# Kernel optimization log

Measured on AMD Instinct MI355X. Metric: run time of the kernel, lower is better.

The kernel has to match this reference:

```python
import jax, jax.numpy as jnp
import numpy as np
import math

B, S = 1, 2048
HID = 4096
NH = 32            # total query heads
NKV = 8            # total kv heads
D = HID // NH      # 128 head_dim
WIN = 1024         # sliding window (layer_idx=1 is odd and < num_layers//2)
LAYER = 1
THETA = 10000.0
LAMBDA_INIT = 0.8 - 0.6 * math.exp(-0.3 * LAYER)
SCALE = D ** -0.5
EPS = 1e-5
OP = NH * D + 2 * NKV * D  # Wqkv output size


def setup_inputs() -> dict:
    key = jax.random.key(0)
    ks = jax.random.split(key, 9)
    std = 0.02
    return {
        "hidden_states": jax.random.normal(ks[0], (B * S, HID), jnp.float32),
        "positions": jnp.tile(jnp.arange(S, dtype=jnp.int32), B),
        "Wqkv_w": jax.random.normal(ks[1], (OP, HID), jnp.float32) * std,
        "Wqkv_b": jnp.zeros((OP,), jnp.float32),
        "out_w": jax.random.normal(ks[2], (HID, NH * D), jnp.float32) * std,
        "out_b": jnp.zeros((HID,), jnp.float32),
        "lambda_q1": jax.random.normal(ks[3], (D,), jnp.float32) * 0.1,
        "lambda_k1": jax.random.normal(ks[4], (D,), jnp.float32) * 0.1,
        "lambda_q2": jax.random.normal(ks[5], (D,), jnp.float32) * 0.1,
        "lambda_k2": jax.random.normal(ks[6], (D,), jnp.float32) * 0.1,
        "subln_w": jnp.ones((2 * D,), jnp.float32),
    }


def _rope(x, pos):
    # neox-style rotary; x: [N, H, D], pos: [N]
    half = D // 2
    inv_freq = 1.0 / (THETA ** (jnp.arange(half, dtype=jnp.float32) / half))
    ang = pos.astype(jnp.float32)[:, None] * inv_freq[None, :]      # [N, half]
    cos = jnp.cos(ang)[:, None, :]
    sin = jnp.sin(ang)[:, None, :]
    x1, x2 = x[..., :half], x[..., half:]
    return jnp.concatenate([x1 * cos - x2 * sin, x2 * cos + x1 * sin], axis=-1)


def _probs(q, k, mask):
    # q: [B,S,Hq,D], k: [B,S,Hkv,D] -> softmax probs [B,Hq,S,S] with GQA repeat
    g = q.shape[2] // k.shape[2]
    k = jnp.repeat(k, g, axis=2)
    scores = jnp.einsum('bqhd,bkhd->bhqk', q, k) * SCALE
    scores = jnp.where(mask, scores, -1e30)
    return jax.nn.softmax(scores, axis=-1)


def _pv(p, v, g):
    # p: [B,Hq,S,S], v: [B,S,Hkv,D]
    v = jnp.repeat(v, g, axis=2)
    return jnp.einsum('bhqk,bkhd->bqhd', p, v)


def reference(hidden_states, positions, Wqkv_w, Wqkv_b, out_w, out_b,
              lambda_q1, lambda_k1, lambda_q2, lambda_k2, subln_w):
    qkv = hidden_states @ Wqkv_w.T + Wqkv_b                 # [N, OP]
    q, k, v = jnp.split(qkv, [NH * D, NH * D + NKV * D], axis=-1)
    q = q.reshape(-1, NH, D)
    k = k.reshape(-1, NKV, D)
    v = v.reshape(-1, NKV, D)
    q = _rope(q, positions)
    k = _rope(k, positions)

    q = q.reshape(B, S, NH, D)
    k = k.reshape(B, S, NKV, D)
    v = v.reshape(B, S, NKV, D)
    # split_heads: '(H two) D' -> even heads = group1, odd heads = group2
    q1, q2 = q[:, :, 0::2], q[:, :, 1::2]
    k1, k2 = k[:, :, 0::2], k[:, :, 1::2]
    v1, v2 = v[:, :, 0::2], v[:, :, 1::2]

    i = jnp.arange(S)[:, None]
    j = jnp.arange(S)[None, :]
    mask = (j <= i) & ((i - j) < WIN)                        # causal + sliding window

    g = (NH // 2) // (NKV // 2)
    p1 = _probs(q1, k1, mask)
    p2 = _probs(q2, k2, mask)
    a11 = _pv(p1, v1, g)
    a12 = _pv(p1, v2, g)
    a21 = _pv(p2, v1, g)
    a22 = _pv(p2, v2, g)

    attn1 = jnp.concatenate([a11, a12], axis=-1)             # [B,S,NH/2,2D]
    attn2 = jnp.concatenate([a21, a22], axis=-1)

    lam = (jnp.exp(jnp.sum(lambda_q1 * lambda_k1))
           - jnp.exp(jnp.sum(lambda_q2 * lambda_k2)) + LAMBDA_INIT)
    attn = attn1 - lam * attn2

    # subln: RMSNorm over last dim (2*head_dim)
    var = jnp.mean(attn * attn, axis=-1, keepdims=True)
    attn = attn * jax.lax.rsqrt(var + EPS) * subln_w
    attn = attn * (1.0 - LAMBDA_INIT)

    attn = attn.reshape(B * S, NH * D)
    return attn @ out_w.T + out_b
```

## Files before the change

### kernel.cpp

```cpp
#include <hip/hip_runtime.h>

typedef unsigned short u16;
typedef __attribute__((ext_vector_type(8))) short bf16x8;
typedef __attribute__((ext_vector_type(4))) float f32x4;
typedef __attribute__((ext_vector_type(4))) unsigned short us4;
typedef __attribute__((ext_vector_type(8))) unsigned short us8;

#define S_LEN 2048
#define QKV_P 6144
#define WIN_SZ 1024
#define SCALE_F 0.08838834764831845f
#define LAMBDA_INIT_F 0.35550906759096925f
#define ONE_MINUS_LI_F 0.6444909324090308f

__device__ __forceinline__ u16 f2bf(float f) {
    union { float f; unsigned int u; } v; v.f = f;
    unsigned int u = v.u;
    return (u16)((u + 0x7fffu + ((u >> 16) & 1u)) >> 16);
}
__device__ __forceinline__ float bf2f(u16 u) {
    union { unsigned int u; float f; } v; v.u = ((unsigned int)u) << 16; return v.f;
}
__device__ __forceinline__ void gload16(const void* g, void* l) {
    __builtin_amdgcn_global_load_lds(
        (const __attribute__((address_space(1))) unsigned int*)g,
        (__attribute__((address_space(3))) unsigned int*)l, 16, 0, 0);
}

__global__ __launch_bounds__(256)
void conv_f32_bf16(const float* __restrict__ src, u16* __restrict__ dst, int n4) {
    for (int i = blockIdx.x * 256 + threadIdx.x; i < n4; i += gridDim.x * 256) {
        float4 v = ((const float4*)src)[i];
        us4 h;
        h.x = f2bf(v.x); h.y = f2bf(v.y); h.z = f2bf(v.z); h.w = f2bf(v.w);
        ((us4*)dst)[i] = h;
    }
}

template<int NR>
__device__ __forceinline__ void stage_half(const u16* __restrict__ src, int K,
                                           int gRowBase, int kcol0,
                                           u16* slot, int tid, int wid) {
#pragma unroll
    for (int g = 0; g < 2; ++g) {
        if (g * 128 + wid * 16 < NR) {
            int row = g * 128 + (tid >> 2);
            int cc = (tid & 3) ^ ((row >> 1) & 3);
            gload16(src + (size_t)(gRowBase + row) * K + kcol0 + cc * 8,
                    slot + g * 4096 + wid * 512);
        }
    }
}

__device__ __forceinline__ bf16x8 ldfrag(const u16* slot, int row, int l4) {
    int pc = l4 ^ ((row >> 1) & 3);
    return *(const bf16x8*)(slot + row * 32 + pc * 8);
}

template<int NF>
__device__ __forceinline__ void gemm_wait(int wid) {
    if constexpr (NF == 3) {
        if (wid < 4) asm volatile("s_waitcnt vmcnt(4)" ::: "memory");
        else         asm volatile("s_waitcnt vmcnt(3)" ::: "memory");
    } else if constexpr (NF == 2) {
        asm volatile("s_waitcnt vmcnt(3)" ::: "memory");
    } else {
        asm volatile("s_waitcnt vmcnt(4)" ::: "memory");
    }
}

template<int NF, int OUT_BF16>
__global__ __launch_bounds__(512)
__attribute__((amdgpu_waves_per_eu(2, 2)))
void gemm8p(const u16* __restrict__ A, const u16* __restrict__ W,
            const float* __restrict__ bias, void* __restrict__ Cv,
            int M, int N, int K, int nbx) {
    constexpr int BN = NF * 64;
    constexpr int BSLOT = NF * 2048;
    __shared__ u16 lds[32768 + 4 * BSLOT];

    const int tid = threadIdx.x;
    const int wid = tid >> 6, lane = tid & 63;
    const int wr = wid >> 2, wc = wid & 3;
    const int l15 = lane & 15, l4 = lane >> 4;

    const int nwg = gridDim.x;
    const int q8 = nwg >> 3;
    const int swz = (blockIdx.x & 7) * q8 + (blockIdx.x >> 3);
    const int bx = swz % nbx, by = swz / nbx;
    const int rowBase = by * 256;
    const int colBase = bx * BN;

    const int NT = K >> 6;

    u16* const baseA = lds;
    u16* const baseB = lds + 32768;

    f32x4 acc[8][NF] = {};

    stage_half<256>(A, K, rowBase, 0,  baseA + 0 * 8192, tid, wid);
    stage_half<BN> (W, K, colBase, 0,  baseB + 0 * BSLOT, tid, wid);
    stage_half<256>(A, K, rowBase, 32, baseA + 1 * 8192, tid, wid);
    stage_half<BN> (W, K, colBase, 32, baseB + 1 * BSLOT, tid, wid);
    stage_half<256>(A, K, rowBase, 64, baseA + 2 * 8192, tid, wid);
    stage_half<BN> (W, K, colBase, 64, baseB + 2 * BSLOT, tid, wid);
    gemm_wait<NF>(wid);
    __builtin_amdgcn_s_barrier();

    for (int t = 0; t < NT; ++t) {
        const int b = t & 1;
        const int bn = b ^ 1;
        u16* const A0 = baseA + (b * 2 + 0) * 8192;
        u16* const A1 = baseA + (b * 2 + 1) * 8192;
        u16* const B0 = baseB + (b * 2 + 0) * BSLOT;
        u16* const B1 = baseB + (b * 2 + 1) * BSLOT;

        bf16x8 af[4], bfv[NF];

#pragma unroll
        for (int m = 0; m < 4; ++m) af[m] = ldfrag(A0, wr * 128 + m * 16 + l15, l4);
#pragma unroll
        for (int n = 0; n < NF; ++n) bfv[n] = ldfrag(B0, wc * (NF * 16) + n * 16 + l15, l4);
        if (t + 1 < NT)
            stage_half<256>(A, K, rowBase, (t + 1) * 64 + 32, baseA + (bn * 2 + 1) * 8192, tid, wid);
        __builtin_amdgcn_s_barrier();
        __builtin_amdgcn_s_setprio(1);
#pragma unroll
        for (int m = 0; m < 4; ++m)
#pragma unroll
            for (int n = 0; n < NF; ++n)
                acc[m][n] = __builtin_amdgcn_mfma_f32_16x16x32_bf16(af[m], bfv[n], acc[m][n], 0, 0, 0);
        __builtin_amdgcn_s_setprio(0);
        __builtin_amdgcn_s_barrier();

#pragma unroll
        for (int m = 0; m < 4; ++m) af[m] = ldfrag(A0, wr * 128 + (m + 4) * 16 + l15, l4);
        if (t + 1 < NT)
            stage_half<BN>(W, K, colBase, (t + 1) * 64 + 32, baseB + (bn * 2 + 1) * BSLOT, tid, wid);
        __builtin_amdgcn_s_barrier();
        __builtin_amdgcn_s_setprio(1);
#pragma unroll
        for (int m = 0; m < 4; ++m)
#pragma unroll
            for (int n = 0; n < NF; ++n)
                acc[m + 4][n] = __builtin_amdgcn_mfma_f32_16x16x32_bf16(af[m], bfv[n], acc[m + 4][n], 0, 0, 0);
        __builtin_amdgcn_s_setprio(0);
        __builtin_amdgcn_s_barrier();

#pragma unroll
        for (int m = 0; m < 4; ++m) af[m] = ldfrag(A1, wr * 128 + m * 16 + l15, l4);
#pragma unroll
        for (int n = 0; n < NF; ++n) bfv[n] = ldfrag(B1, wc * (NF * 16) + n * 16 + l15, l4);
        if (t + 2 < NT)
            stage_half<256>(A, K, rowBase, (t + 2) * 64, baseA + (b * 2 + 0) * 8192, tid, wid);
        __builtin_amdgcn_s_barrier();
        __builtin_amdgcn_s_setprio(1);
#pragma unroll
        for (int m = 0; m < 4; ++m)
#pragma unroll
            for (int n = 0; n < NF; ++n)
                acc[m][n] = __builtin_amdgcn_mfma_f32_16x16x32_bf16(af[m], bfv[n], acc[m][n], 0, 0, 0);
        __builtin_amdgcn_s_setprio(0);
        __builtin_amdgcn_s_barrier();

#pragma unroll
        for (int m = 0; m < 4; ++m) af[m] = ldfrag(A1, wr * 128 + (m + 4) * 16 + l15, l4);
        if (t + 2 < NT)
            stage_half<BN>(W, K, colBase, (t + 2) * 64, baseB + (b * 2 + 0) * BSLOT, tid, wid);
        __builtin_amdgcn_s_barrier();
        __builtin_amdgcn_s_setprio(1);
#pragma unroll
        for (int m = 0; m < 4; ++m)
#pragma unroll
            for (int n = 0; n < NF; ++n)
                acc[m + 4][n] = __builtin_amdgcn_mfma_f32_16x16x32_bf16(af[m], bfv[n], acc[m + 4][n], 0, 0, 0);
        __builtin_amdgcn_s_setprio(0);
        if (t + 2 < NT) gemm_wait<NF>(wid);
        else            asm volatile("s_waitcnt vmcnt(0)" ::: "memory");
        __builtin_amdgcn_s_barrier();
    }

#pragma unroll
    for (int n = 0; n < NF; ++n) {
        int col = colBase + wc * (NF * 16) + n * 16 + l15;
        float bs = bias[col];
#pragma unroll
        for (int m = 0; m < 8; ++m)
#pragma unroll
            for (int rr = 0; rr < 4; ++rr) {
                int rowi = rowBase + wr * 128 + m * 16 + l4 * 4 + rr;
                float v = acc[m][n][rr] + bs;
                if (OUT_BF16) ((u16*)Cv)[(size_t)rowi * N + col] = f2bf(v);
                else          ((float*)Cv)[(size_t)rowi * N + col] = v;
            }
    }
}

__global__ __launch_bounds__(256)
void rope_bf16(u16* __restrict__ qkv, const int* __restrict__ positions) {
    const int row = blockIdx.x;
    const float pos = (float)positions[row];
    for (int idx = threadIdx.x; idx < 640; idx += 256) {
        int head = idx >> 4;
        int g = idx & 15;
        int base = (head < 32) ? head * 128 : 4096 + (head - 32) * 128;
        u16* p = qkv + (size_t)row * QKV_P + base + g * 4;
        us4 x1 = *(us4*)p;
        us4 x2 = *(us4*)(p + 64);
#pragma unroll
        for (int j = 0; j < 4; ++j) {
            float inv_freq = __expf(-(float)(g * 4 + j) * (9.210340371976184f / 64.0f));
            float ang = pos * inv_freq;
            float s, c;
            sincosf(ang, &s, &c);
            float a = bf2f(x1[j]), b = bf2f(x2[j]);
            x1[j] = f2bf(a * c - b * s);
            x2[j] = f2bf(b * c + a * s);
        }
        *(us4*)p = x1;
        *(us4*)(p + 64) = x2;
    }
}

__global__ __launch_bounds__(256)
void vtrans(const u16* __restrict__ qkv, u16* __restrict__ vt) {
    __shared__ u16 T[128 * 72];
    const int s0 = blockIdx.x * 64;
    const int a = blockIdx.y;
    const u16* src = qkv + 5120 + a * 128;
#pragma unroll
    for (int it = 0; it < 4; ++it) {
        int idx = it * 256 + threadIdx.x;
        int s = idx >> 4;
        int c8 = idx & 15;
        us8 v = *(const us8*)(src + (size_t)(s0 + s) * QKV_P + c8 * 8);
        int sc = s >> 3, su = s & 7;
#pragma unroll
        for (int j = 0; j < 8; ++j) {
            int d = c8 * 8 + j;
            T[d * 72 + ((sc ^ ((d >> 3) & 7)) * 8 + su)] = v[j];
        }
    }
    __syncthreads();
#pragma unroll
    for (int it = 0; it < 4; ++it) {
        int idx = it * 256 + threadIdx.x;
        int d = idx >> 3, sc = idx & 7;
        us8 v = *(const us8*)&T[d * 72 + ((sc ^ ((d >> 3) & 7)) * 8)];
        *(us8*)(vt + (size_t)a * 262144 + (size_t)d * 2048 + s0 + sc * 8) = v;
    }
}

__global__ __launch_bounds__(512)
__attribute__((amdgpu_waves_per_eu(2, 2)))
void attn_bf16(const u16* __restrict__ qkv, const u16* __restrict__ vtg,
               u16* __restrict__ attnb,
               const float* __restrict__ lq1, const float* __restrict__ lk1,
               const float* __restrict__ lq2, const float* __restrict__ lk2,
               const float* __restrict__ subln) {
    __shared__ u16 smem[73728];
#define KBUF(b, st) (smem + ((b) * 2 + (st)) * 8192)
#define VBUF(b, st) (smem + 32768 + ((b) * 2 + (st)) * 8192)

    const int tid = threadIdx.x;
    const int w = tid >> 6, lane = tid & 63;
    const int g = w & 3, sid = w >> 2;
    const int l15 = lane & 15, l4 = lane >> 4;
    u16* const Pw = smem + 65536 + w * 1024;

    int qb, h;
    {
        int i = blockIdx.x;
        if (i < 256) { qb = 16 + (i & 15); h = i >> 4; }
        else         { int j = i - 256; qb = j & 15; h = j >> 4; }
    }
    const int q0 = qb * 64;
    const int a1 = 2 * (h >> 2), a2 = a1 + 1;

    bf16x8 qf[4];
    {
        int qrow = q0 + g * 16 + l15;
        const u16* qp = qkv + (size_t)qrow * QKV_P + (2 * h + sid) * 128;
#pragma unroll
        for (int kk = 0; kk < 4; ++kk)
            qf[kk] = *(const bf16x8*)(qp + kk * 32 + l4 * 8);
    }

    f32x4 aV1[8] = {}, aV2[8] = {};
    float m[4], l[4];
#pragma unroll
    for (int r = 0; r < 4; ++r) { m[r] = -1e30f; l[r] = 0.f; }

    const int kr4 = lane >> 4, kc = lane & 15;
    const int vd8 = lane >> 3, vc = lane & 7;

    const int tbeg = (qb >= 16) ? (qb - 16) : 0;
    const int tend = qb;

#define STAGE_TILE(T, NB)                                                      \
    {                                                                          \
        const int kv0s = (T) * 64;                                             \
        _Pragma("unroll")                                                      \
        for (int s2 = 0; s2 < 2; ++s2) {                                       \
            int ch = w * 2 + s2;                                               \
            int krow = ch * 4 + kr4;                                           \
            int kcs = (kc ^ (krow & 7)) * 8;                                   \
            const u16* kbase = qkv + (size_t)(kv0s + krow) * QKV_P + 4096;     \
            gload16(kbase + a1 * 128 + kcs, KBUF(NB, 0) + ch * 512);           \
            gload16(kbase + a2 * 128 + kcs, KBUF(NB, 1) + ch * 512);           \
            int vdrow = ch * 8 + vd8;                                          \
            int vcs = (vc ^ (vdrow & 7)) * 8;                                  \
            const u16* vbase = vtg + (size_t)vdrow * 2048 + kv0s + vcs;        \
            gload16(vbase + (size_t)a1 * 262144, VBUF(NB, 0) + ch * 512);      \
            gload16(vbase + (size_t)a2 * 262144, VBUF(NB, 1) + ch * 512);      \
        }                                                                      \
    }

    STAGE_TILE(tbeg, 0);
    asm volatile("s_waitcnt vmcnt(0)" ::: "memory");
    __builtin_amdgcn_s_barrier();
    asm volatile("" ::: "memory");

    int cb = 0;
    for (int t = tbeg; t <= tend; ++t) {
        const int kv0 = t * 64;

        if (t < tend) STAGE_TILE(t + 1, cb ^ 1);

        f32x4 sc[4];
        const u16* Kc = KBUF(cb, sid);
        __builtin_amdgcn_s_setprio(1);
#pragma unroll
        for (int c = 0; c < 4; ++c) {
            f32x4 s1 = {0.f, 0.f, 0.f, 0.f};
#pragma unroll
            for (int kk = 0; kk < 4; ++kk) {
                int off = (c * 16 + l15) * 128 + (((kk * 4 + l4) ^ (l15 & 7)) * 8);
                s1 = __builtin_amdgcn_mfma_f32_16x16x32_bf16(qf[kk], *(const bf16x8*)&Kc[off], s1, 0, 0, 0);
            }
            sc[c] = s1;
        }
        __builtin_amdgcn_s_setprio(0);

        const bool dz = (t == tend);
        const bool wz = (qb >= 16) && (t <= tbeg + 1);
        if (dz) {
#pragma unroll
            for (int c = 0; c < 4; ++c) {
                int j = kv0 + c * 16 + l15;
#pragma unroll
                for (int r = 0; r < 4; ++r) {
                    int i = q0 + g * 16 + l4 * 4 + r;
                    if (j > i) sc[c][r] = -1e30f;
                }
            }
        } else if (wz) {
#pragma unroll
            for (int c = 0; c < 4; ++c) {
                int j = kv0 + c * 16 + l15;
#pragma unroll
                for (int r = 0; r < 4; ++r) {
                    int i = q0 + g * 16 + l4 * 4 + r;
                    if (i - j >= WIN_SZ) sc[c][r] = -1e30f;
                }
            }
        }

        float rmax[4];
#pragma unroll
        for (int r = 0; r < 4; ++r)
            rmax[r] = fmaxf(fmaxf(sc[0][r], sc[1][r]), fmaxf(sc[2][r], sc[3][r]));
#pragma unroll
        for (int msk = 1; msk < 16; msk <<= 1)
#pragma unroll
            for (int r = 0; r < 4; ++r)
                rmax[r] = fmaxf(rmax[r], __shfl_xor(rmax[r], msk));
        bool need = false;
#pragma unroll
        for (int r = 0; r < 4; ++r)
            need = need || (rmax[r] > m[r] + 32.0f);
        if (__any(need)) {
            float fr[4];
#pragma unroll
            for (int r = 0; r < 4; ++r) {
                float nm = fmaxf(m[r], rmax[r]);
                fr[r] = __expf((m[r] - nm) * SCALE_F);
                m[r] = nm;
                l[r] *= fr[r];
            }
#pragma unroll
            for (int f = 0; f < 8; ++f)
#pragma unroll
                for (int r = 0; r < 4; ++r) {
                    aV1[f][r] *= fr[r];
                    aV2[f][r] *= fr[r];
                }
        }

        float rs[4] = {0.f, 0.f, 0.f, 0.f};
#pragma unroll
        for (int c = 0; c < 4; ++c) {
            int col = c * 16 + l15;
#pragma unroll
            for (int r = 0; r < 4; ++r) {
                int prow = l4 * 4 + r;
                float p = __expf((sc[c][r] - m[r]) * SCALE_F);
                if (wz && (m[r] < -1e29f)) p = 0.f;
                rs[r] += p;
                int pco = ((col >> 3) ^ (prow & 7)) * 8 + (col & 7);
                Pw[prow * 64 + pco] = f2bf(p);
            }
        }
#pragma unroll
        for (int msk = 1; msk < 16; msk <<= 1)
#pragma unroll
            for (int r = 0; r < 4; ++r)
                rs[r] += __shfl_xor(rs[r], msk);
#pragma unroll
        for (int r = 0; r < 4; ++r) l[r] += rs[r];

        const u16* V0 = VBUF(cb, 0);
        const u16* V1 = VBUF(cb, 1);
        __builtin_amdgcn_s_setprio(1);
#pragma unroll
        for (int kk = 0; kk < 2; ++kk) {
            int pch = ((kk * 4 + l4) ^ (l15 & 7)) * 8;
            bf16x8 pa = *(const bf16x8*)&Pw[l15 * 64 + pch];
#pragma unroll
            for (int f = 0; f < 8; ++f) {
                int off = (f * 16 + l15) * 64 + (((kk * 4 + l4) ^ (l15 & 7)) * 8);
                aV1[f] = __builtin_amdgcn_mfma_f32_16x16x32_bf16(pa, *(const bf16x8*)&V0[off], aV1[f], 0, 0, 0);
                aV2[f] = __builtin_amdgcn_mfma_f32_16x16x32_bf16(pa, *(const bf16x8*)&V1[off], aV2[f], 0, 0, 0);
            }
        }
        __builtin_amdgcn_s_setprio(0);

        asm volatile("s_waitcnt vmcnt(0)" ::: "memory");
        __builtin_amdgcn_s_barrier();
        asm volatile("" ::: "memory");
        cb ^= 1;
    }

    float s1v = lq1[lane] * lk1[lane] + lq1[lane + 64] * lk1[lane + 64];
    float s2v = lq2[lane] * lk2[lane] + lq2[lane + 64] * lk2[lane + 64];
#pragma unroll
    for (int msk = 1; msk < 64; msk <<= 1) {
        s1v += __shfl_xor(s1v, msk);
        s2v += __shfl_xor(s2v, msk);
    }
    const float lam = __expf(s1v) - __expf(s2v) + LAMBDA_INIT_F;

    float* const Cmb = (float*)smem;
    if (sid == 1) {
#pragma unroll
        for (int r = 0; r < 4; ++r) {
            float inv2 = lam / l[r];
            int row = g * 16 + l4 * 4 + r;
#pragma unroll
            for (int f = 0; f < 8; ++f) {
                Cmb[row * 264 + f * 16 + l15]       = aV1[f][r] * inv2;
                Cmb[row * 264 + 128 + f * 16 + l15] = aV2[f][r] * inv2;
            }
        }
    }
    __syncthreads();
    if (sid == 0) {
        float sw0[8], sw1[8];
#pragma unroll
        for (int f = 0; f < 8; ++f) {
            sw0[f] = subln[f * 16 + l15];
            sw1[f] = subln[128 + f * 16 + l15];
        }
#pragma unroll
        for (int r = 0; r < 4; ++r) {
            float inv1 = 1.0f / l[r];
            int row = g * 16 + l4 * 4 + r;
            float o0[8], o1[8];
            float ssq = 0.f;
#pragma unroll
            for (int f = 0; f < 8; ++f) {
                o0[f] = aV1[f][r] * inv1 - Cmb[row * 264 + f * 16 + l15];
                o1[f] = aV2[f][r] * inv1 - Cmb[row * 264 + 128 + f * 16 + l15];
                ssq += o0[f] * o0[f] + o1[f] * o1[f];
            }
#pragma unroll
            for (int msk = 1; msk < 16; msk <<= 1) ssq += __shfl_xor(ssq, msk);
            float scale = rsqrtf(ssq * (1.0f / 256.0f) + 1e-5f) * ONE_MINUS_LI_F;
            u16* op = attnb + (size_t)(q0 + row) * 4096 + h * 256;
#pragma unroll
            for (int f = 0; f < 8; ++f) {
                op[f * 16 + l15]       = f2bf(o0[f] * scale * sw0[f]);
                op[128 + f * 16 + l15] = f2bf(o1[f] * scale * sw1[f]);
            }
        }
    }
#undef STAGE_TILE
#undef KBUF
#undef VBUF
}

extern "C" void kernel_launch(void* const* d_in, const int* in_sizes, int n_in,
                              void* d_out, int out_size, void* d_ws, size_t ws_size,
                              hipStream_t stream) {
    const float* hidden    = (const float*)d_in[0];
    const int*   positions = (const int*)d_in[1];
    const float* Wqkv_w    = (const float*)d_in[2];
    const float* Wqkv_b    = (const float*)d_in[3];
    const float* out_w     = (const float*)d_in[4];
    const float* out_b     = (const float*)d_in[5];
    const float* lq1       = (const float*)d_in[6];
    const float* lk1       = (const float*)d_in[7];
    const float* lq2       = (const float*)d_in[8];
    const float* lk2       = (const float*)d_in[9];
    const float* subln     = (const float*)d_in[10];
    float* out = (float*)d_out;

    u16* ws0   = (u16*)d_ws;
    u16* hb    = ws0;
    u16* wqb   = ws0 + 8388608;
    u16* qkvb  = ws0 + 33554432;
    u16* attnb = ws0;
    u16* owb   = ws0 + 8388608;
    u16* vt    = ws0 + 25165824;

    conv_f32_bf16<<<2048, 256, 0, stream>>>(hidden, hb, 2048 * 4096 / 4);
    conv_f32_bf16<<<2048, 256, 0, stream>>>(Wqkv_w, wqb, 6144 * 4096 / 4);

    gemm8p<3, 1><<<256, 512, 0, stream>>>(hb, wqb, Wqkv_b, qkvb, 2048, 6144, 4096, 32);

    rope_bf16<<<S_LEN, 256, 0, stream>>>(qkvb, positions);
    vtrans<<<dim3(32, 8), 256, 0, stream>>>(qkvb, vt);

    conv_f32_bf16<<<2048, 256, 0, stream>>>(out_w, owb, 4096 * 4096 / 4);

    attn_bf16<<<512, 512, 0, stream>>>(qkvb, vt, attnb, lq1, lk1, lq2, lk2, subln);

    gemm8p<2, 0><<<256, 512, 0, stream>>>(attnb, owb, out_b, out, 2048, 4096, 4096, 32);
}
```

Baseline: 362.9 us.

## Halve attention KV tile to 32 rows to cut LDS and raise occupancy

Shrinks the KV tile processed per iteration from 64 to 32 keys. This halves the shared-memory footprint (K/V double buffers and P scratch) and drops the fixed two-waves-per-EU attribute, so more workgroups can be resident per CU. The LDS swizzle patterns, staging addresses, mask boundaries and PV loop are reworked for the narrower tile. In exchange the loop runs twice as many iterations, each with its own barrier, online-softmax reductions and waits.

```diff
diff --git a/kernel.cpp b/kernel.cpp
--- a/kernel.cpp
+++ b/kernel.cpp
@@ -252,21 +252,20 @@
 }
 
 __global__ __launch_bounds__(512)
-__attribute__((amdgpu_waves_per_eu(2, 2)))
 void attn_bf16(const u16* __restrict__ qkv, const u16* __restrict__ vtg,
                u16* __restrict__ attnb,
                const float* __restrict__ lq1, const float* __restrict__ lk1,
                const float* __restrict__ lq2, const float* __restrict__ lk2,
                const float* __restrict__ subln) {
-    __shared__ u16 smem[73728];
-#define KBUF(b, st) (smem + ((b) * 2 + (st)) * 8192)
-#define VBUF(b, st) (smem + 32768 + ((b) * 2 + (st)) * 8192)
+    __shared__ u16 smem[36864];
+#define KBUF(b, st) (smem + ((b) * 2 + (st)) * 4096)
+#define VBUF(b, st) (smem + 16384 + ((b) * 2 + (st)) * 4096)
 
     const int tid = threadIdx.x;
     const int w = tid >> 6, lane = tid & 63;
     const int g = w & 3, sid = w >> 2;
     const int l15 = lane & 15, l4 = lane >> 4;
-    u16* const Pw = smem + 65536 + w * 1024;
+    u16* const Pw = smem + 32768 + w * 512;
 
     int qb, h;
     {
@@ -291,29 +290,25 @@
 #pragma unroll
     for (int r = 0; r < 4; ++r) { m[r] = -1e30f; l[r] = 0.f; }
 
-    const int kr4 = lane >> 4, kc = lane & 15;
-    const int vd8 = lane >> 3, vc = lane & 7;
-
-    const int tbeg = (qb >= 16) ? (qb - 16) : 0;
-    const int tend = qb;
+    const int krow = w * 4 + (lane >> 4);
+    const int kcs  = ((lane & 15) ^ (krow & 7)) * 8;
+    const int vd   = w * 16 + (lane >> 2);
+    const int vcs  = ((lane & 3) ^ ((vd & 3) ^ ((vd >> 2) & 3))) * 8;
+
+    const int rsw = (l15 & 3) ^ (l15 >> 2);
+
+    const int tend = 2 * qb + 1;
+    const int tbeg = (qb >= 16) ? (2 * qb - 32) : 0;
 
 #define STAGE_TILE(T, NB)                                                      \
     {                                                                          \
-        const int kv0s = (T) * 64;                                             \
-        _Pragma("unroll")                                                      \
-        for (int s2 = 0; s2 < 2; ++s2) {                                       \
-            int ch = w * 2 + s2;                                               \
-            int krow = ch * 4 + kr4;                                           \
-            int kcs = (kc ^ (krow & 7)) * 8;                                   \
-            const u16* kbase = qkv + (size_t)(kv0s + krow) * QKV_P + 4096;     \
-            gload16(kbase + a1 * 128 + kcs, KBUF(NB, 0) + ch * 512);           \
-            gload16(kbase + a2 * 128 + kcs, KBUF(NB, 1) + ch * 512);           \
-            int vdrow = ch * 8 + vd8;                                          \
-            int vcs = (vc ^ (vdrow & 7)) * 8;                                  \
-            const u16* vbase = vtg + (size_t)vdrow * 2048 + kv0s + vcs;        \
-            gload16(vbase + (size_t)a1 * 262144, VBUF(NB, 0) + ch * 512);      \
-            gload16(vbase + (size_t)a2 * 262144, VBUF(NB, 1) + ch * 512);      \
-        }                                                                      \
+        const int kv0s = (T) * 32;                                             \
+        const u16* kbase = qkv + (size_t)(kv0s + krow) * QKV_P + 4096;         \
+        gload16(kbase + a1 * 128 + kcs, KBUF(NB, 0) + w * 512);                \
+        gload16(kbase + a2 * 128 + kcs, KBUF(NB, 1) + w * 512);                \
+        const u16* vbase = vtg + (size_t)vd * 2048 + kv0s + vcs;               \
+        gload16(vbase + (size_t)a1 * 262144, VBUF(NB, 0) + w * 512);           \
+        gload16(vbase + (size_t)a2 * 262144, VBUF(NB, 1) + w * 512);           \
     }
 
     STAGE_TILE(tbeg, 0);
@@ -323,15 +318,15 @@
 
     int cb = 0;
     for (int t = tbeg; t <= tend; ++t) {
-        const int kv0 = t * 64;
+        const int kv0 = t * 32;
 
         if (t < tend) STAGE_TILE(t + 1, cb ^ 1);
 
-        f32x4 sc[4];
+        f32x4 sc[2];
         const u16* Kc = KBUF(cb, sid);
         __builtin_amdgcn_s_setprio(1);
 #pragma unroll
-        for (int c = 0; c < 4; ++c) {
+        for (int c = 0; c < 2; ++c) {
             f32x4 s1 = {0.f, 0.f, 0.f, 0.f};
 #pragma unroll
             for (int kk = 0; kk < 4; ++kk) {
@@ -342,11 +337,11 @@
         }
         __builtin_amdgcn_s_setprio(0);
 
-        const bool dz = (t == tend);
+        const bool dz = (t >= tend - 1);
         const bool wz = (qb >= 16) && (t <= tbeg + 1);
         if (dz) {
 #pragma unroll
-            for (int c = 0; c < 4; ++c) {
+            for (int c = 0; c < 2; ++c) {
                 int j = kv0 + c * 16 + l15;
 #pragma unroll
                 for (int r = 0; r < 4; ++r) {
@@ -356,7 +351,7 @@
             }
         } else if (wz) {
 #pragma unroll
-            for (int c = 0; c < 4; ++c) {
+            for (int c = 0; c < 2; ++c) {
                 int j = kv0 + c * 16 + l15;
 #pragma unroll
                 for (int r = 0; r < 4; ++r) {
@@ -369,7 +364,7 @@
         float rmax[4];
 #pragma unroll
         for (int r = 0; r < 4; ++r)
-            rmax[r] = fmaxf(fmaxf(sc[0][r], sc[1][r]), fmaxf(sc[2][r], sc[3][r]));
+            rmax[r] = fmaxf(sc[0][r], sc[1][r]);
 #pragma unroll
         for (int msk = 1; msk < 16; msk <<= 1)
 #pragma unroll
@@ -399,16 +394,17 @@
 
         float rs[4] = {0.f, 0.f, 0.f, 0.f};
 #pragma unroll
-        for (int c = 0; c < 4; ++c) {
+        for (int c = 0; c < 2; ++c) {
             int col = c * 16 + l15;
+            int pc8 = col >> 3;
 #pragma unroll
             for (int r = 0; r < 4; ++r) {
                 int prow = l4 * 4 + r;
                 float p = __expf((sc[c][r] - m[r]) * SCALE_F);
                 if (wz && (m[r] < -1e29f)) p = 0.f;
                 rs[r] += p;
-                int pco = ((col >> 3) ^ (prow & 7)) * 8 + (col & 7);
-                Pw[prow * 64 + pco] = f2bf(p);
+                int phys = pc8 ^ ((prow & 3) ^ ((prow >> 2) & 3));
+                Pw[prow * 32 + phys * 8 + (col & 7)] = f2bf(p);
             }
         }
 #pragma unroll
@@ -421,17 +417,14 @@
 
         const u16* V0 = VBUF(cb, 0);
         const u16* V1 = VBUF(cb, 1);
+        const int chnk = (l4 ^ rsw) * 8;
+        bf16x8 pa = *(const bf16x8*)&Pw[l15 * 32 + chnk];
         __builtin_amdgcn_s_setprio(1);
 #pragma unroll
-        for (int kk = 0; kk < 2; ++kk) {
-            int pch = ((kk * 4 + l4) ^ (l15 & 7)) * 8;
-            bf16x8 pa = *(const bf16x8*)&Pw[l15 * 64 + pch];
-#pragma unroll
-            for (int f = 0; f < 8; ++f) {
-                int off = (f * 16 + l15) * 64 + (((kk * 4 + l4) ^ (l15 & 7)) * 8);
-                aV1[f] = __builtin_amdgcn_mfma_f32_16x16x32_bf16(pa, *(const bf16x8*)&V0[off], aV1[f], 0, 0, 0);
-                aV2[f] = __builtin_amdgcn_mfma_f32_16x16x32_bf16(pa, *(const bf16x8*)&V1[off], aV2[f], 0, 0, 0);
-            }
+        for (int f = 0; f < 8; ++f) {
+            int off = (f * 16 + l15) * 32 + chnk;
+            aV1[f] = __builtin_amdgcn_mfma_f32_16x16x32_bf16(pa, *(const bf16x8*)&V0[off], aV1[f], 0, 0, 0);
+            aV2[f] = __builtin_amdgcn_mfma_f32_16x16x32_bf16(pa, *(const bf16x8*)&V1[off], aV2[f], 0, 0, 0);
         }
         __builtin_amdgcn_s_setprio(0);
 
```

New measurement: 398.8 us. 9.9% more time.
